# Optimization experiments

Measured on AMD Instinct MI355X. Metric: run time of the kernel, lower is better.

## Reference

```python
import jax, jax.numpy as jnp
import numpy as np

N, L, D = 16, 128, 128
H, C = 8, 16
EPS = 1e-5


def setup_inputs() -> dict:
    key = jax.random.key(0)
    ks = jax.random.split(key, 10)
    s = 0.02
    return {
        "z": jax.random.normal(ks[0], (N, L, L, D), dtype=jnp.float32),
        "ln_w": jnp.ones((D,), jnp.float32),
        "ln_b": jnp.zeros((D,), jnp.float32),
        "Wq": jax.random.normal(ks[1], (D, H * C), jnp.float32) * s,
        "Wk": jax.random.normal(ks[2], (D, H * C), jnp.float32) * s,
        "Wv": jax.random.normal(ks[3], (D, H * C), jnp.float32) * s,
        "Wg": jax.random.normal(ks[4], (D, H * C), jnp.float32) * s,
        "bg": jnp.zeros((H * C,), jnp.float32),
        "Wo": jax.random.normal(ks[5], (H * C, D), jnp.float32) * s,
        "bo": jnp.zeros((D,), jnp.float32),
    }


def reference(z, ln_w, ln_b, Wq, Wk, Wv, Wg, bg, Wo, bo):
    n, l, _, d = z.shape
    # LayerNorm over channel dim
    mu = jnp.mean(z, axis=-1, keepdims=True)
    var = jnp.var(z, axis=-1, keepdims=True)
    zn = (z - mu) * jax.lax.rsqrt(var + EPS) * ln_w + ln_b
    # projections -> (N, L, L, H, C)
    q = (zn @ Wq).reshape(n, l, l, H, C)
    k = (zn @ Wk).reshape(n, l, l, H, C)
    v = (zn @ Wv).reshape(n, l, l, H, C)
    g = jax.nn.sigmoid(zn @ Wg + bg).reshape(n, l, l, H, C)
    # attention over the sample axis N, per pair position (a,b) and head h
    att = jnp.einsum('iabhc,jabhc->ijabh', q, k) * (1.0 / np.sqrt(C))
    att = jax.nn.softmax(att, axis=1)
    o = jnp.einsum('ijabh,jabhc->iabhc', att, v) * g
    out = o.reshape(n, l, l, H * C) @ Wo + bo
    return out
```

## Files before the change

kernel.cpp:

```cpp
#include <hip/hip_runtime.h>
#include <hip/hip_bf16.h>


typedef short bf16x8 __attribute__((ext_vector_type(8)));
typedef float f32x4 __attribute__((ext_vector_type(4)));

#define MFMA16x32(A, B, C) __builtin_amdgcn_mfma_f32_16x16x32_bf16((A), (B), (C), 0, 0, 0)

__device__ __forceinline__ unsigned short f2bf(float f) {
    unsigned int u = __float_as_uint(f);
    u += 0x7fffu + ((u >> 16) & 1u);
    return (unsigned short)(u >> 16);
}

static constexpr int  DD     = 128;
static constexpr int  NPOS   = 128 * 128;
static constexpr long ZSTR   = (long)NPOS * DD;
static constexpr int  ZN_STR = 136;
static constexpr int  SB_STR = 56;
static constexpr int  OB_STR = 132;

__launch_bounds__(256, 2)
__global__ void ssattn_fused(const float* __restrict__ z,
                             const float* __restrict__ ln_w,
                             const float* __restrict__ ln_b,
                             const float* __restrict__ Wq,
                             const float* __restrict__ Wk,
                             const float* __restrict__ Wv,
                             const float* __restrict__ Wg,
                             const float* __restrict__ bg,
                             const float* __restrict__ Wo,
                             const float* __restrict__ bo,
                             float* __restrict__ out)
{
    __shared__ __align__(16) unsigned short zn_s[16 * ZN_STR];
    __shared__ __align__(16) unsigned short ob_s[16 * ZN_STR];
    __shared__ __align__(16) float outb_s[16 * OB_STR];
    __shared__ __align__(16) unsigned short qb_s[4][16 * SB_STR];
    __shared__ __align__(16) unsigned short kq_s[4][16 * SB_STR];
    __shared__ __align__(16) unsigned short vb_s[4][16 * SB_STR];
    __shared__ float lnw_s[DD];
    __shared__ float lnb_s[DD];

    const int tid  = threadIdx.x;
    const int wid  = tid >> 6;
    const int lane = tid & 63;
    const int quad = lane >> 4;
    const int lm   = lane & 15;
    const int r16  = tid >> 4;
    const int s16  = tid & 15;

    if (tid < DD) { lnw_s[tid] = ln_w[tid]; lnb_s[tid] = ln_b[tid]; }
    for (int i = tid; i < 16 * SB_STR; i += 256) {
        qb_s[0][i] = 0; qb_s[1][i] = 0; qb_s[2][i] = 0; qb_s[3][i] = 0;
        kq_s[0][i] = 0; kq_s[1][i] = 0; kq_s[2][i] = 0; kq_s[3][i] = 0;
        vb_s[0][i] = 0; vb_s[1][i] = 0; vb_s[2][i] = 0; vb_s[3][i] = 0;
    }

    bf16x8 wq_r[2][4], wk_r[2][4], wv_r[2][4], wg_r[2][4], wo_r[2][4];
    float bg_r[2], bo_r[2];
#pragma unroll
    for (int hl = 0; hl < 2; ++hl) {
        const int col = (wid * 2 + hl) * 16 + lm;
        bg_r[hl] = bg[col];
        bo_r[hl] = bo[col];
#pragma unroll
        for (int kb = 0; kb < 4; ++kb) {
            const int kbase = kb * 32 + quad * 8;
            bf16x8 a, b, c, d, e;
#pragma unroll
            for (int j = 0; j < 8; ++j) {
                const int k = kbase + j;
                a[j] = (short)f2bf(Wq[k * DD + col]);
                b[j] = (short)f2bf(Wk[k * DD + col]);
                c[j] = (short)f2bf(Wv[k * DD + col]);
                d[j] = (short)f2bf(Wg[k * DD + col]);
                e[j] = (short)f2bf(Wo[k * DD + col]);
            }
            wq_r[hl][kb] = a; wk_r[hl][kb] = b; wv_r[hl][kb] = c;
            wg_r[hl][kb] = d; wo_r[hl][kb] = e;
        }
    }
    __syncthreads();

    unsigned short* const qb = qb_s[wid];
    unsigned short* const kq = kq_s[wid];
    unsigned short* const vb = vb_s[wid];

    for (int p = blockIdx.x; p < NPOS; p += gridDim.x) {
        {
            const float* zp = z + (long)r16 * ZSTR + (long)p * DD + s16 * 8;
            const float4 ra = *(const float4*)zp;
            const float4 rb = *(const float4*)(zp + 4);
            float x[8] = {ra.x, ra.y, ra.z, ra.w, rb.x, rb.y, rb.z, rb.w};
            float s = 0.f, ss = 0.f;
#pragma unroll
            for (int j = 0; j < 8; ++j) { s += x[j]; ss += x[j] * x[j]; }
#pragma unroll
            for (int m = 1; m <= 8; m <<= 1) {
                s  += __shfl_xor(s,  m, 16);
                ss += __shfl_xor(ss, m, 16);
            }
            const float mu = s * (1.f / 128.f);
            const float rs = rsqrtf(ss * (1.f / 128.f) - mu * mu + 1e-5f);
            unsigned int pk[4];
#pragma unroll
            for (int jj = 0; jj < 4; ++jj) {
                const int c0 = s16 * 8 + jj * 2;
                const unsigned short lo = f2bf((x[jj * 2]     - mu) * rs * lnw_s[c0]     + lnb_s[c0]);
                const unsigned short hi = f2bf((x[jj * 2 + 1] - mu) * rs * lnw_s[c0 + 1] + lnb_s[c0 + 1]);
                pk[jj] = (unsigned)lo | ((unsigned)hi << 16);
            }
            uint4 st; st.x = pk[0]; st.y = pk[1]; st.z = pk[2]; st.w = pk[3];
            *(uint4*)&zn_s[r16 * ZN_STR + s16 * 8] = st;
        }
        __syncthreads();

        bf16x8 af[4];
#pragma unroll
        for (int kb = 0; kb < 4; ++kb)
            af[kb] = *(const bf16x8*)&zn_s[lm * ZN_STR + kb * 32 + quad * 8];

#pragma unroll
        for (int hl = 0; hl < 2; ++hl) {
            f32x4 aq = {0,0,0,0}, ak = {0,0,0,0}, av = {0,0,0,0}, ag = {0,0,0,0};
#pragma unroll
            for (int kb = 0; kb < 4; ++kb) {
                aq = MFMA16x32(af[kb], wq_r[hl][kb], aq);
                ak = MFMA16x32(af[kb], wk_r[hl][kb], ak);
                av = MFMA16x32(af[kb], wv_r[hl][kb], av);
                ag = MFMA16x32(af[kb], wg_r[hl][kb], ag);
            }
#pragma unroll
            for (int r = 0; r < 4; ++r) {
                const int row = quad * 4 + r;
                qb[row * SB_STR + lm] = f2bf(aq[r] * 0.25f);
                kq[row * SB_STR + lm] = f2bf(ak[r]);
                vb[lm * SB_STR + row] = f2bf(av[r]);
            }
            float gv[4];
#pragma unroll
            for (int r = 0; r < 4; ++r)
                gv[r] = 1.f / (1.f + __expf(-(ag[r] + bg_r[hl])));

            const bf16x8 aqf = *(const bf16x8*)&qb[lm * SB_STR + quad * 8];
            const bf16x8 bkf = *(const bf16x8*)&kq[lm * SB_STR + quad * 8];
            const f32x4 z4 = {0,0,0,0};
            f32x4 att = MFMA16x32(aqf, bkf, z4);

            f32x4 pr;
#pragma unroll
            for (int r = 0; r < 4; ++r) {
                const float a = att[r];
                float mx = a;
#pragma unroll
                for (int m = 1; m <= 8; m <<= 1) mx = fmaxf(mx, __shfl_xor(mx, m, 16));
                const float ex = __expf(a - mx);
                float sm = ex;
#pragma unroll
                for (int m = 1; m <= 8; m <<= 1) sm += __shfl_xor(sm, m, 16);
                pr[r] = ex / sm;
            }
#pragma unroll
            for (int r = 0; r < 4; ++r)
                qb[(quad * 4 + r) * SB_STR + lm] = f2bf(pr[r]);

            const bf16x8 apf = *(const bf16x8*)&qb[lm * SB_STR + quad * 8];
            const bf16x8 bvf = *(const bf16x8*)&vb[lm * SB_STR + quad * 8];
            f32x4 oc = MFMA16x32(apf, bvf, z4);

            const int hcol = (wid * 2 + hl) * 16 + lm;
#pragma unroll
            for (int r = 0; r < 4; ++r)
                ob_s[(quad * 4 + r) * ZN_STR + hcol] = f2bf(oc[r] * gv[r]);
        }
        __syncthreads();

        bf16x8 of[4];
#pragma unroll
        for (int kb = 0; kb < 4; ++kb)
            of[kb] = *(const bf16x8*)&ob_s[lm * ZN_STR + kb * 32 + quad * 8];
#pragma unroll
        for (int hl = 0; hl < 2; ++hl) {
            f32x4 acc = {0,0,0,0};
#pragma unroll
            for (int kb = 0; kb < 4; ++kb)
                acc = MFMA16x32(of[kb], wo_r[hl][kb], acc);
            const int col = (wid * 2 + hl) * 16 + lm;
#pragma unroll
            for (int r = 0; r < 4; ++r)
                outb_s[(quad * 4 + r) * OB_STR + col] = acc[r] + bo_r[hl];
        }
        __syncthreads();

        {
            float* op = out + (long)r16 * ZSTR + (long)p * DD + s16 * 8;
            const float* sp = &outb_s[r16 * OB_STR + s16 * 8];
            float4 v0 = *(const float4*)(sp);
            float4 v1 = *(const float4*)(sp + 4);
            *(float4*)(op)     = v0;
            *(float4*)(op + 4) = v1;
        }
        __syncthreads();
    }
}

extern "C" void kernel_launch(void* const* d_in, const int* in_sizes, int n_in,
                              void* d_out, int out_size, void* d_ws, size_t ws_size,
                              hipStream_t stream) {
    (void)in_sizes; (void)n_in; (void)out_size; (void)d_ws; (void)ws_size;
    ssattn_fused<<<dim3(512), dim3(256), 0, stream>>>(
        (const float*)d_in[0],
        (const float*)d_in[1],
        (const float*)d_in[2],
        (const float*)d_in[3],
        (const float*)d_in[4],
        (const float*)d_in[5],
        (const float*)d_in[6],
        (const float*)d_in[7],
        (const float*)d_in[8],
        (const float*)d_in[9],
        (float*)d_out);
}
```

Before: 342.0 us.

## Prefetch next z tile into registers and store output directly from MFMA

The kernel now loads the next position's z slice into registers right after the LayerNorm barrier, so the global read latency overlaps the projection, attention and output MFMA work of the current position. It also drops the outb_s shared staging buffer and its two barriers, writing each accumulator element straight to global memory from the MFMA layout. This cuts shared memory use and per-iteration synchronisation. The cost is narrower, scalar 64-byte-segment stores instead of float4 writes, plus one redundant load on the final iteration.

```diff
diff --git a/kernel.cpp b/kernel.cpp
--- a/kernel.cpp
+++ b/kernel.cpp
@@ -18,7 +18,6 @@
 static constexpr long ZSTR   = (long)NPOS * DD;
 static constexpr int  ZN_STR = 136;
 static constexpr int  SB_STR = 56;
-static constexpr int  OB_STR = 132;
 
 __launch_bounds__(256, 2)
 __global__ void ssattn_fused(const float* __restrict__ z,
@@ -35,7 +34,6 @@
 {
     __shared__ __align__(16) unsigned short zn_s[16 * ZN_STR];
     __shared__ __align__(16) unsigned short ob_s[16 * ZN_STR];
-    __shared__ __align__(16) float outb_s[16 * OB_STR];
     __shared__ __align__(16) unsigned short qb_s[4][16 * SB_STR];
     __shared__ __align__(16) unsigned short kq_s[4][16 * SB_STR];
     __shared__ __align__(16) unsigned short vb_s[4][16 * SB_STR];
@@ -87,12 +85,17 @@
     unsigned short* const kq = kq_s[wid];
     unsigned short* const vb = vb_s[wid];
 
-    for (int p = blockIdx.x; p < NPOS; p += gridDim.x) {
+    int p = blockIdx.x;
+    float4 cura, curb;
+    {
+        const float* zp = z + (long)r16 * ZSTR + (long)p * DD + s16 * 8;
+        cura = *(const float4*)zp;
+        curb = *(const float4*)(zp + 4);
+    }
+
+    for (; p < NPOS; p += gridDim.x) {
         {
-            const float* zp = z + (long)r16 * ZSTR + (long)p * DD + s16 * 8;
-            const float4 ra = *(const float4*)zp;
-            const float4 rb = *(const float4*)(zp + 4);
-            float x[8] = {ra.x, ra.y, ra.z, ra.w, rb.x, rb.y, rb.z, rb.w};
+            float x[8] = {cura.x, cura.y, cura.z, cura.w, curb.x, curb.y, curb.z, curb.w};
             float s = 0.f, ss = 0.f;
 #pragma unroll
             for (int j = 0; j < 8; ++j) { s += x[j]; ss += x[j] * x[j]; }
@@ -116,6 +119,14 @@
         }
         __syncthreads();
 
+        {
+            const int pn  = p + gridDim.x;
+            const int pnc = (pn < NPOS) ? pn : p;
+            const float* zp2 = z + (long)r16 * ZSTR + (long)pnc * DD + s16 * 8;
+            cura = *(const float4*)zp2;
+            curb = *(const float4*)(zp2 + 4);
+        }
+
         bf16x8 af[4];
 #pragma unroll
         for (int kb = 0; kb < 4; ++kb)
@@ -180,6 +191,7 @@
 #pragma unroll
         for (int kb = 0; kb < 4; ++kb)
             of[kb] = *(const bf16x8*)&ob_s[lm * ZN_STR + kb * 32 + quad * 8];
+        float* const op0 = out + (long)p * DD + (long)(quad * 4) * ZSTR;
 #pragma unroll
         for (int hl = 0; hl < 2; ++hl) {
             f32x4 acc = {0,0,0,0};
@@ -189,19 +201,8 @@
             const int col = (wid * 2 + hl) * 16 + lm;
 #pragma unroll
             for (int r = 0; r < 4; ++r)
-                outb_s[(quad * 4 + r) * OB_STR + col] = acc[r] + bo_r[hl];
-        }
-        __syncthreads();
-
-        {
-            float* op = out + (long)r16 * ZSTR + (long)p * DD + s16 * 8;
-            const float* sp = &outb_s[r16 * OB_STR + s16 * 8];
-            float4 v0 = *(const float4*)(sp);
-            float4 v1 = *(const float4*)(sp + 4);
-            *(float4*)(op)     = v0;
-            *(float4*)(op + 4) = v1;
-        }
-        __syncthreads();
+                op0[(long)r * ZSTR + col] = acc[r] + bo_r[hl];
+        }
     }
 }
 
```

Result: faster. 319.7 us (-6.5%).
